# Kernel optimization log

Hardware: AMD Instinct MI355X
Metric: run time of the kernel (lower is better)

Reference implementation:

```python
import jax, jax.numpy as jnp
import numpy as np

HEADS = 16
LN_EPS = 1e-5


def setup_inputs() -> dict:
    key = jax.random.key(0)
    ks = jax.random.split(key, 12)
    B, IMG, Q, H = 8192, 2048, 768, 1024
    def init(k, shape, fan_in):
        return jax.random.normal(k, shape, dtype=jnp.float32) * (fan_in ** -0.5)
    return {
        "features1": jax.random.normal(ks[0], (B, IMG), dtype=jnp.float32),
        "features2": jax.random.normal(ks[1], (B, Q), dtype=jnp.float32),
        "W1": init(ks[2], (IMG, H), IMG),
        "b1": jnp.zeros((H,), dtype=jnp.float32),
        "W2": init(ks[3], (Q, H), Q),
        "b2": jnp.zeros((H,), dtype=jnp.float32),
        "Wqkv": init(ks[4], (H, 3 * H), H),
        "Wout": init(ks[5], (H, H), H),
        "bout": jnp.zeros((H,), dtype=jnp.float32),
        "gamma": jnp.ones((2 * H,), dtype=jnp.float32),
        "beta": jnp.zeros((2 * H,), dtype=jnp.float32),
    }


def reference(features1, features2, W1, b1, W2, b2, Wqkv, Wout, bout, gamma, beta):
    B = features1.shape[0]
    H = W1.shape[1]
    hd = H // HEADS
    scale = hd ** -0.5
    # modality projections -> [B, H] each
    f1 = features1 @ W1 + b1
    f2 = features2 @ W2 + b2
    x = jnp.stack([f1, f2], axis=1)                      # [B, 2, H]
    qkv = x @ Wqkv                                       # [B, 2, 3H]
    q, k, v = jnp.split(qkv, 3, axis=-1)
    # b n (h d) -> b h n d
    def to_heads(t):
        return t.reshape(B, 2, HEADS, hd).transpose(0, 2, 1, 3)
    q, k, v = to_heads(q) * scale, to_heads(k), to_heads(v)
    attn = jnp.einsum('bhid,bhjd->bhij', q, k)           # [B, h, 2, 2]
    attn = jax.nn.softmax(attn, axis=-1)
    out = jnp.einsum('bhij,bhjd->bhid', attn, v)         # [B, h, 2, d]
    out = out.transpose(0, 2, 1, 3).reshape(B, 2, H)     # b h n d -> b n (h d)
    out = out @ Wout + bout                              # [B, 2, H]
    flat = out.reshape(B, 2 * H)
    # LayerNorm over last dim
    mu = jnp.mean(flat, axis=-1, keepdims=True)
    var = jnp.var(flat, axis=-1, keepdims=True)
    normed = (flat - mu) * jax.lax.rsqrt(var + LN_EPS) * gamma + beta
    # dropout in eval mode = identity
    res = jnp.concatenate([f1, f2], axis=1)              # [B, 2H]
    return normed + res
```

## Files before the change

kernel.cpp:

```cpp
#include <hip/hip_runtime.h>
#include <hip/hip_bf16.h>
#include <cstdint>

typedef __attribute__((ext_vector_type(8))) short short8;
typedef __attribute__((ext_vector_type(4))) short short4v;
typedef __attribute__((ext_vector_type(4))) float floatx4;
typedef __attribute__((ext_vector_type(4))) unsigned short ushort4v;

__device__ __forceinline__ float bf2f(unsigned short u) {
    union { unsigned int u; float f; } v;
    v.u = ((unsigned int)u) << 16;
    return v.f;
}
__device__ __forceinline__ unsigned short f2bf(float f) {
    union { float f; unsigned int u; } v; v.f = f;
    unsigned int u = v.u;
    unsigned int r = (u + 0x7FFFu + ((u >> 16) & 1u)) >> 16;
    return (unsigned short)r;
}
__device__ __forceinline__ float lo_bf(unsigned int u) {
    union { unsigned int u; float f; } v; v.u = u << 16; return v.f;
}
__device__ __forceinline__ float hi_bf(unsigned int u) {
    union { unsigned int u; float f; } v; v.u = u & 0xffff0000u; return v.f;
}
__device__ __forceinline__ void gld_lds16(const void* g, void* l) {
    __builtin_amdgcn_global_load_lds(
        (const __attribute__((address_space(1))) unsigned int*)g,
        (__attribute__((address_space(3))) unsigned int*)l,
        16, 0, 0);
}

__global__ __launch_bounds__(256) void prep_kernel(
    const float* __restrict__ f1, const float* __restrict__ f2,
    unsigned short* __restrict__ f1b, unsigned short* __restrict__ f2b,
    const float* __restrict__ W1, unsigned short* __restrict__ W1t,
    const float* __restrict__ W2, unsigned short* __restrict__ W2t,
    const float* __restrict__ Wqkv, unsigned short* __restrict__ Wqkvt,
    const float* __restrict__ Wout, unsigned short* __restrict__ Woutt) {
    __shared__ float tile[64][33];
    const int b = blockIdx.x;
    const int tid = threadIdx.x;

    if (b < 5632) {
        const float* in = (b < 4096) ? f1 : f2;
        unsigned short* outp = (b < 4096) ? f1b : f2b;
        int base = ((b < 4096) ? b : (b - 4096)) * 1024 + tid;
#pragma unroll
        for (int it = 0; it < 4; it++) {
            int i = base + it * 256;
            float4 v = ((const float4*)in)[i];
            ushort4v o;
            o.x = f2bf(v.x); o.y = f2bf(v.y); o.z = f2bf(v.z); o.w = f2bf(v.w);
            ((ushort4v*)outp)[i] = o;
        }
        return;
    }

    const float* in; unsigned short* outp; int K, N, t;
    if (b < 6656)      { in = W1;   outp = W1t;   K = 2048; N = 1024; t = b - 5632; }
    else if (b < 7040) { in = W2;   outp = W2t;   K = 768;  N = 1024; t = b - 6656; }
    else if (b < 8576) { in = Wqkv; outp = Wqkvt; K = 1024; N = 3072; t = b - 7040; }
    else               { in = Wout; outp = Woutt; K = 1024; N = 1024; t = b - 8576; }
    const int ntiles = N >> 5;
    const int n0 = (t % ntiles) * 32;
    const int k0 = (t / ntiles) * 64;
    const int tx = tid & 31, tg = tid >> 5;
#pragma unroll
    for (int i = 0; i < 8; i++)
        tile[tg * 8 + i][tx] = in[(size_t)(k0 + tg * 8 + i) * N + n0 + tx];
    __syncthreads();
    const int n = tid >> 3, kc = (tid & 7) * 8;
    short8 o;
#pragma unroll
    for (int j = 0; j < 8; j++) o[j] = (short)f2bf(tile[kc + j][n]);
    *(short8*)&outp[(size_t)(n0 + n) * K + k0 + kc] = o;
}

template <bool OUT_BF16, bool HAS_BIAS>
__device__ __forceinline__ void gemm_core(const unsigned short* __restrict__ A,
                                          const unsigned short* __restrict__ Bt,
                                          void* __restrict__ Cv, const float* __restrict__ bias,
                                          int K, int ldc, int blockM, int blockN,
                                          unsigned short* As, unsigned short* Bs) {
    const int tid  = threadIdx.x;
    const int lane = tid & 63;
    const int wave = tid >> 6;
    const int wm = wave >> 1, wn = wave & 1;

    const int kx = (tid >> 3) & 3;
    const unsigned short* gA = A  + (size_t)(blockM + (tid >> 2)) * K + ((tid & 3) ^ kx) * 8;
    const unsigned short* gB = Bt + (size_t)(blockN + (tid >> 2)) * K + ((tid & 3) ^ kx) * 8;
    const size_t sK = (size_t)64 * K;
    unsigned short* lA = As + wave * 512;
    unsigned short* lB = Bs + wave * 512;

    floatx4 acc[4][4];
#pragma unroll
    for (int i = 0; i < 4; i++)
#pragma unroll
        for (int j = 0; j < 4; j++) acc[i][j] = (floatx4){0.f, 0.f, 0.f, 0.f};

    const int col  = lane & 15;
    const int quad = lane >> 4;
    const int qx = quad ^ ((col >> 1) & 3);
    const int aoff32 = (wm * 64 + col) * 32 + qx * 8;
    const int boff32 = (wn * 64 + col) * 32 + qx * 8;

    const int kIters = K >> 6;
    for (int kt = 0; kt < kIters; ++kt) {
        const size_t ko = (size_t)kt * 64;
        gld_lds16(gA + ko,           lA);
        gld_lds16(gA + sK + ko,      lA + 2048);
        gld_lds16(gA + 32 + ko,      lA + 4096);
        gld_lds16(gA + sK + 32 + ko, lA + 6144);
        gld_lds16(gB + ko,           lB);
        gld_lds16(gB + sK + ko,      lB + 2048);
        gld_lds16(gB + 32 + ko,      lB + 4096);
        gld_lds16(gB + sK + 32 + ko, lB + 6144);
        __syncthreads();

#pragma unroll
        for (int hh = 0; hh < 2; hh++) {
            short8 a[4];
#pragma unroll
            for (int i = 0; i < 4; i++) a[i] = *(const short8*)&As[hh * 4096 + aoff32 + i * 512];
#pragma unroll
            for (int j = 0; j < 4; j++) {
                short8 bj = *(const short8*)&Bs[hh * 4096 + boff32 + j * 512];
#pragma unroll
                for (int i = 0; i < 4; i++)
                    acc[i][j] = __builtin_amdgcn_mfma_f32_16x16x32_bf16(a[i], bj, acc[i][j], 0, 0, 0);
            }
        }
        __syncthreads();
    }

#pragma unroll
    for (int i = 0; i < 4; i++) {
#pragma unroll
        for (int j = 0; j < 4; j++) {
#pragma unroll
            for (int r = 0; r < 4; r++) {
                int row = blockM + wm * 64 + i * 16 + quad * 4 + r;
                int cn  = blockN + wn * 64 + j * 16 + col;
                float v = acc[i][j][r];
                if (HAS_BIAS) v += bias[cn];
                if (OUT_BF16) ((unsigned short*)Cv)[(size_t)row * ldc + cn] = f2bf(v);
                else          ((float*)Cv)[(size_t)row * ldc + cn] = v;
            }
        }
    }
}

__global__ __launch_bounds__(256, 3)
void gemm_f12(const unsigned short* __restrict__ f1b, const unsigned short* __restrict__ W1t,
              const float* __restrict__ b1,
              const unsigned short* __restrict__ f2b, const unsigned short* __restrict__ W2t,
              const float* __restrict__ b2, unsigned short* __restrict__ xb) {
    __shared__ alignas(16) unsigned short As[8192];
    __shared__ alignas(16) unsigned short Bs[8192];
    const int blockM = blockIdx.x * 128;
    const int blockN = blockIdx.y * 128;
    if (blockIdx.z == 0)
        gemm_core<true, true>(f1b, W1t, (void*)xb, b1, 2048, 2048, blockM, blockN, As, Bs);
    else
        gemm_core<true, true>(f2b, W2t, (void*)(xb + 1024), b2, 768, 2048, blockM, blockN, As, Bs);
}

__global__ __launch_bounds__(256, 3)
void gemm_proj(const unsigned short* __restrict__ attn, const unsigned short* __restrict__ Woutt,
               const float* __restrict__ bout, unsigned short* __restrict__ projb) {
    __shared__ alignas(16) unsigned short As[8192];
    __shared__ alignas(16) unsigned short Bs[8192];
    gemm_core<true, true>(attn, Woutt, (void*)projb, bout, 1024, 1024,
                          blockIdx.x * 128, blockIdx.y * 128, As, Bs);
}

#define QKV_LDS_BYTES 116736
#define T2_ST 264
__global__ __launch_bounds__(512, 2)
void gemm_qkv_attn2(const unsigned short* __restrict__ A, const unsigned short* __restrict__ Bt,
                    unsigned short* __restrict__ attn_out) {
    extern __shared__ __align__(16) char smem[];
    unsigned short* buf0 = (unsigned short*)smem;
    unsigned short* buf1 = (unsigned short*)(smem + 57344);
    unsigned short* T2   = (unsigned short*)smem;
    float* wsm = (float*)(smem + 114688);

    const int tid  = threadIdx.x;
    const int lane = tid & 63;
    const int wave = tid >> 6;
    const int wm = wave >> 1;
    const int wn = wave & 1;
    const int g = blockIdx.x;
    const int h = g >> 6;
    const int blockM = (g & 63) * 256;
    const int K = 1024;

    const int srow = tid >> 3;
    const int schunk = (tid & 7) ^ (srow & 7);
    const unsigned short* gA = A  + (size_t)(blockM + srow) * K + schunk * 8;
    const unsigned short* gB = Bt + (size_t)(h * 64 + srow) * K + schunk * 8;
    const int sdst = wave * 512;

#define STAGE_A(bufp, koff) do { \
    gld_lds16(gA + (koff),          (bufp) + sdst);          \
    gld_lds16(gA + 65536 + (koff),  (bufp) + 4096 + sdst);   \
    gld_lds16(gA + 131072 + (koff), (bufp) + 8192 + sdst);   \
    gld_lds16(gA + 196608 + (koff), (bufp) + 12288 + sdst); } while (0)
#define STAGE_B(bufp, koff) do { \
    gld_lds16(gB + (koff),           (bufp) + 16384 + sdst);         \
    gld_lds16(gB + 1048576 + (koff), (bufp) + 16384 + 4096 + sdst);  \
    gld_lds16(gB + 2097152 + (koff), (bufp) + 16384 + 8192 + sdst); } while (0)

    floatx4 acc[4][6];
#pragma unroll
    for (int i = 0; i < 4; i++)
#pragma unroll
        for (int j = 0; j < 6; j++) acc[i][j] = (floatx4){0.f, 0.f, 0.f, 0.f};

    const int col  = lane & 15;
    const int quad = lane >> 4;
    const int ch0  = (quad ^ (col & 7)) * 8;
    int aoff[4], boff[6];
#pragma unroll
    for (int i = 0; i < 4; i++) aoff[i] = (wm * 64 + i * 16 + col) * 64 + ch0;
#pragma unroll
    for (int j = 0; j < 6; j++) boff[j] = 16384 + (wn * 96 + j * 16 + col) * 64 + ch0;

    STAGE_A(buf0, 0);
    STAGE_B(buf0, 0);

    for (int kt = 0; kt < 16; ++kt) {
        unsigned short* cur = (kt & 1) ? buf1 : buf0;
        unsigned short* nxt = (kt & 1) ? buf0 : buf1;
        const int kn = (kt + 1) * 64;
        __syncthreads();

        short8 a0[4], b0v[3];
#pragma unroll
        for (int i = 0; i < 4; i++) a0[i] = *(const short8*)&cur[aoff[i]];
#pragma unroll
        for (int j = 0; j < 3; j++) b0v[j] = *(const short8*)&cur[boff[j]];
        if (kt < 15) { STAGE_A(nxt, kn); }
        __builtin_amdgcn_sched_barrier(0);
        __builtin_amdgcn_s_barrier();
        asm volatile("s_waitcnt lgkmcnt(0)" ::: "memory");
        __builtin_amdgcn_sched_barrier(0);
        __builtin_amdgcn_s_setprio(1);
#pragma unroll
        for (int j = 0; j < 3; j++)
#pragma unroll
            for (int i = 0; i < 4; i++)
                acc[i][j] = __builtin_amdgcn_mfma_f32_16x16x32_bf16(a0[i], b0v[j], acc[i][j], 0, 0, 0);
        __builtin_amdgcn_s_setprio(0);
        __builtin_amdgcn_sched_barrier(0);
        __builtin_amdgcn_s_barrier();

        short8 b1v[3];
#pragma unroll
        for (int j = 0; j < 3; j++) b1v[j] = *(const short8*)&cur[boff[3 + j]];
        if (kt < 15) { STAGE_B(nxt, kn); }
        __builtin_amdgcn_sched_barrier(0);
        __builtin_amdgcn_s_barrier();
        asm volatile("s_waitcnt lgkmcnt(0)" ::: "memory");
        __builtin_amdgcn_sched_barrier(0);
        __builtin_amdgcn_s_setprio(1);
#pragma unroll
        for (int j = 0; j < 3; j++)
#pragma unroll
            for (int i = 0; i < 4; i++)
                acc[i][3 + j] = __builtin_amdgcn_mfma_f32_16x16x32_bf16(a0[i], b1v[j], acc[i][3 + j], 0, 0, 0);
        __builtin_amdgcn_s_setprio(0);
        __builtin_amdgcn_sched_barrier(0);
        __builtin_amdgcn_s_barrier();

        short8 a1[4], b2v[3];
#pragma unroll
        for (int i = 0; i < 4; i++) a1[i] = *(const short8*)&cur[aoff[i] ^ 32];
#pragma unroll
        for (int j = 0; j < 3; j++) b2v[j] = *(const short8*)&cur[boff[j] ^ 32];
        __builtin_amdgcn_sched_barrier(0);
        __builtin_amdgcn_s_barrier();
        asm volatile("s_waitcnt lgkmcnt(0)" ::: "memory");
        __builtin_amdgcn_sched_barrier(0);
        __builtin_amdgcn_s_setprio(1);
#pragma unroll
        for (int j = 0; j < 3; j++)
#pragma unroll
            for (int i = 0; i < 4; i++)
                acc[i][j] = __builtin_amdgcn_mfma_f32_16x16x32_bf16(a1[i], b2v[j], acc[i][j], 0, 0, 0);
        __builtin_amdgcn_s_setprio(0);
        __builtin_amdgcn_sched_barrier(0);
        __builtin_amdgcn_s_barrier();

        short8 b3v[3];
#pragma unroll
        for (int j = 0; j < 3; j++) b3v[j] = *(const short8*)&cur[boff[3 + j] ^ 32];
        __builtin_amdgcn_sched_barrier(0);
        __builtin_amdgcn_s_barrier();
        asm volatile("s_waitcnt lgkmcnt(0)" ::: "memory");
        __builtin_amdgcn_sched_barrier(0);
        __builtin_amdgcn_s_setprio(1);
#pragma unroll
        for (int j = 0; j < 3; j++)
#pragma unroll
            for (int i = 0; i < 4; i++)
                acc[i][3 + j] = __builtin_amdgcn_mfma_f32_16x16x32_bf16(a1[i], b3v[j], acc[i][3 + j], 0, 0, 0);
        __builtin_amdgcn_s_setprio(0);
    }
    __syncthreads();
#undef STAGE_A
#undef STAGE_B

#pragma unroll
    for (int i = 0; i < 4; i++) {
#pragma unroll
        for (int j = 0; j < 6; j++) {
            int c  = wn * 96 + j * 16 + col;
            int r0 = wm * 64 + i * 16 + quad * 4;
            short4v pk;
            pk.x = (short)f2bf(acc[i][j][0]);
            pk.y = (short)f2bf(acc[i][j][1]);
            pk.z = (short)f2bf(acc[i][j][2]);
            pk.w = (short)f2bf(acc[i][j][3]);
            *(short4v*)&T2[c * T2_ST + r0] = pk;
        }
    }
    __syncthreads();

    if (tid < 128) {
        const int ib = tid;
        float s00 = 0.f, s01 = 0.f, s10 = 0.f, s11 = 0.f;
#pragma unroll 8
        for (int d = 0; d < 64; d++) {
            unsigned int qp = *(const unsigned int*)&T2[d * T2_ST + 2 * ib];
            unsigned int kp = *(const unsigned int*)&T2[(64 + d) * T2_ST + 2 * ib];
            float q0 = lo_bf(qp), q1 = hi_bf(qp);
            float k0 = lo_bf(kp), k1 = hi_bf(kp);
            s00 += q0 * k0; s01 += q0 * k1;
            s10 += q1 * k0; s11 += q1 * k1;
        }
        const float sc = 0.125f;
        s00 *= sc; s01 *= sc; s10 *= sc; s11 *= sc;
        float m0 = fmaxf(s00, s01), m1 = fmaxf(s10, s11);
        float e00 = __expf(s00 - m0), e01 = __expf(s01 - m0);
        float e10 = __expf(s10 - m1), e11 = __expf(s11 - m1);
        float i0 = 1.f / (e00 + e01), i1 = 1.f / (e10 + e11);
        wsm[ib * 4 + 0] = e00 * i0; wsm[ib * 4 + 1] = e01 * i0;
        wsm[ib * 4 + 2] = e10 * i1; wsm[ib * 4 + 3] = e11 * i1;
    }
    __syncthreads();

#pragma unroll
    for (int gg = 0; gg < 4; gg++) {
        int chunk = gg * 512 + tid;
        int r = chunk >> 3;
        int dc = (chunk & 7) * 8;
        int ib = r >> 1, n = r & 1;
        float w0 = wsm[ib * 4 + n * 2 + 0];
        float w1 = wsm[ib * 4 + n * 2 + 1];
        short8 o;
#pragma unroll
        for (int dd = 0; dd < 8; dd++) {
            unsigned int vp = *(const unsigned int*)&T2[(128 + dc + dd) * T2_ST + 2 * ib];
            o[dd] = (short)f2bf(w0 * lo_bf(vp) + w1 * hi_bf(vp));
        }
        *(short8*)&attn_out[(size_t)(blockM + r) * 1024 + h * 64 + dc] = o;
    }
}

__global__ __launch_bounds__(256) void ln_res_kernel(const unsigned short* __restrict__ proj,
                                                     const unsigned short* __restrict__ xres,
                                                     const float* __restrict__ gamma,
                                                     const float* __restrict__ beta,
                                                     float* __restrict__ out) {
    const int b = blockIdx.x;
    const int tid = threadIdx.x;
    const size_t base = (size_t)b * 2048;
    short8 p8 = ((const short8*)(proj + base))[tid];
    float pv[8];
#pragma unroll
    for (int e = 0; e < 8; e++) pv[e] = bf2f((unsigned short)p8[e]);
    float s = 0.f, ss = 0.f;
#pragma unroll
    for (int e = 0; e < 8; e++) { s += pv[e]; ss += pv[e] * pv[e]; }
#pragma unroll
    for (int off = 32; off > 0; off >>= 1) {
        s  += __shfl_xor(s, off);
        ss += __shfl_xor(ss, off);
    }
    __shared__ float red[8];
    const int wave = tid >> 6;
    if ((tid & 63) == 0) { red[wave] = s; red[4 + wave] = ss; }
    __syncthreads();
    s  = red[0] + red[1] + red[2] + red[3];
    ss = red[4] + red[5] + red[6] + red[7];
    const float mean = s * (1.0f / 2048.0f);
    const float var  = ss * (1.0f / 2048.0f) - mean * mean;
    const float rstd = rsqrtf(var + 1e-5f);

    const float4* g4 = (const float4*)gamma;
    const float4* b4 = (const float4*)beta;
    float4 g0 = g4[2 * tid], g1 = g4[2 * tid + 1];
    float4 be0 = b4[2 * tid], be1 = b4[2 * tid + 1];
    short8 r8 = ((const short8*)(xres + base))[tid];
    float4 o0, o1;
    o0.x = (pv[0] - mean) * rstd * g0.x + be0.x + bf2f((unsigned short)r8[0]);
    o0.y = (pv[1] - mean) * rstd * g0.y + be0.y + bf2f((unsigned short)r8[1]);
    o0.z = (pv[2] - mean) * rstd * g0.z + be0.z + bf2f((unsigned short)r8[2]);
    o0.w = (pv[3] - mean) * rstd * g0.w + be0.w + bf2f((unsigned short)r8[3]);
    o1.x = (pv[4] - mean) * rstd * g1.x + be1.x + bf2f((unsigned short)r8[4]);
    o1.y = (pv[5] - mean) * rstd * g1.y + be1.y + bf2f((unsigned short)r8[5]);
    o1.z = (pv[6] - mean) * rstd * g1.z + be1.z + bf2f((unsigned short)r8[6]);
    o1.w = (pv[7] - mean) * rstd * g1.w + be1.w + bf2f((unsigned short)r8[7]);
    float4* op = (float4*)(out + base);
    op[2 * tid] = o0;
    op[2 * tid + 1] = o1;
}

extern "C" void kernel_launch(void* const* d_in, const int* in_sizes, int n_in,
                              void* d_out, int out_size, void* d_ws, size_t ws_size,
                              hipStream_t stream) {
    (void)in_sizes; (void)n_in; (void)out_size; (void)ws_size;
    const float* features1 = (const float*)d_in[0];
    const float* features2 = (const float*)d_in[1];
    const float* W1   = (const float*)d_in[2];
    const float* b1   = (const float*)d_in[3];
    const float* W2   = (const float*)d_in[4];
    const float* b2   = (const float*)d_in[5];
    const float* Wqkv = (const float*)d_in[6];
    const float* Wout = (const float*)d_in[7];
    const float* bout = (const float*)d_in[8];
    const float* gamma = (const float*)d_in[9];
    const float* beta  = (const float*)d_in[10];
    float* out = (float*)d_out;

    static bool qkv2_init = false;
    if (!qkv2_init) {
        (void)hipFuncSetAttribute((const void*)gemm_qkv_attn2,
                                  hipFuncAttributeMaxDynamicSharedMemorySize,
                                  QKV_LDS_BYTES);
        qkv2_init = true;
    }

    char* ws = (char*)d_ws;
    unsigned short* f1b   = (unsigned short*)(ws);
    unsigned short* f2b   = (unsigned short*)(ws + 33554432);
    unsigned short* W1t   = (unsigned short*)(ws + 46137344);
    unsigned short* W2t   = (unsigned short*)(ws + 50331648);
    unsigned short* Wqkvt = (unsigned short*)(ws + 51904512);
    unsigned short* Woutt = (unsigned short*)(ws + 58195968);
    unsigned short* xb    = (unsigned short*)(ws + 60293120);
    unsigned short* attn  = (unsigned short*)(ws + 93847552);
    unsigned short* projb = (unsigned short*)(ws + 127401984);

    prep_kernel<<<9088, 256, 0, stream>>>(features1, features2, f1b, f2b,
                                          W1, W1t, W2, W2t, Wqkv, Wqkvt, Wout, Woutt);
    gemm_f12<<<dim3(64, 8, 2), 256, 0, stream>>>(f1b, W1t, b1, f2b, W2t, b2, xb);
    gemm_qkv_attn2<<<1024, 512, QKV_LDS_BYTES, stream>>>(xb, Wqkvt, attn);
    gemm_proj<<<dim3(128, 8), 256, 0, stream>>>(attn, Woutt, bout, projb);
    ln_res_kernel<<<8192, 256, 0, stream>>>(projb, xb, gamma, beta, out);
}
```

Measured before the change: 389.1 us.

## Split QKV-attention K tile into halves with finer-grained prefetch and vmcnt waits

The fused QKV+attention GEMM now stores each 64-wide K tile as two 32-wide half-tiles with a new XOR swizzle. Global-to-LDS staging is split into four smaller chunks interleaved across the four MFMA phases, with explicit vmcnt waits replacing the leading __syncthreads. The intent is to overlap global loads with compute more evenly and reduce LDS bank conflicts. LDS grows to 128 KB per block, which with two blocks per CU may exceed capacity and reduce occupancy. The projection GEMMs also raise launch_bounds min-blocks from 3 to 4, which may cause register pressure.

```diff
diff --git a/kernel.cpp b/kernel.cpp
--- a/kernel.cpp
+++ b/kernel.cpp
@@ -153,7 +153,7 @@
     }
 }
 
-__global__ __launch_bounds__(256, 3)
+__global__ __launch_bounds__(256, 4)
 void gemm_f12(const unsigned short* __restrict__ f1b, const unsigned short* __restrict__ W1t,
               const float* __restrict__ b1,
               const unsigned short* __restrict__ f2b, const unsigned short* __restrict__ W2t,
@@ -168,7 +168,7 @@
         gemm_core<true, true>(f2b, W2t, (void*)(xb + 1024), b2, 768, 2048, blockM, blockN, As, Bs);
 }
 
-__global__ __launch_bounds__(256, 3)
+__global__ __launch_bounds__(256, 4)
 void gemm_proj(const unsigned short* __restrict__ attn, const unsigned short* __restrict__ Woutt,
                const float* __restrict__ bout, unsigned short* __restrict__ projb) {
     __shared__ alignas(16) unsigned short As[8192];
@@ -177,42 +177,50 @@
                           blockIdx.x * 128, blockIdx.y * 128, As, Bs);
 }
 
-#define QKV_LDS_BYTES 116736
+#define QKV_LDS_BYTES 131072
 #define T2_ST 264
 __global__ __launch_bounds__(512, 2)
-void gemm_qkv_attn2(const unsigned short* __restrict__ A, const unsigned short* __restrict__ Bt,
+void gemm_qkv_attn8(const unsigned short* __restrict__ A, const unsigned short* __restrict__ Bt,
                     unsigned short* __restrict__ attn_out) {
     extern __shared__ __align__(16) char smem[];
     unsigned short* buf0 = (unsigned short*)smem;
-    unsigned short* buf1 = (unsigned short*)(smem + 57344);
+    unsigned short* buf1 = buf0 + 32768;
     unsigned short* T2   = (unsigned short*)smem;
-    float* wsm = (float*)(smem + 114688);
+    float* wsm = (float*)(smem + 101376);
 
     const int tid  = threadIdx.x;
     const int lane = tid & 63;
     const int wave = tid >> 6;
-    const int wm = wave >> 1;
-    const int wn = wave & 1;
     const int g = blockIdx.x;
     const int h = g >> 6;
     const int blockM = (g & 63) * 256;
+    const int wm = wave >> 1;
+    const int wn = wave & 1;
     const int K = 1024;
 
-    const int srow = tid >> 3;
-    const int schunk = (tid & 7) ^ (srow & 7);
-    const unsigned short* gA = A  + (size_t)(blockM + srow) * K + schunk * 8;
-    const unsigned short* gB = Bt + (size_t)(h * 64 + srow) * K + schunk * 8;
-    const int sdst = wave * 512;
-
-#define STAGE_A(bufp, koff) do { \
-    gld_lds16(gA + (koff),          (bufp) + sdst);          \
-    gld_lds16(gA + 65536 + (koff),  (bufp) + 4096 + sdst);   \
-    gld_lds16(gA + 131072 + (koff), (bufp) + 8192 + sdst);   \
-    gld_lds16(gA + 196608 + (koff), (bufp) + 12288 + sdst); } while (0)
-#define STAGE_B(bufp, koff) do { \
-    gld_lds16(gB + (koff),           (bufp) + 16384 + sdst);         \
-    gld_lds16(gB + 1048576 + (koff), (bufp) + 16384 + 4096 + sdst);  \
-    gld_lds16(gB + 2097152 + (koff), (bufp) + 16384 + 8192 + sdst); } while (0)
+    const int srow = tid >> 2;
+    const int sch  = ((tid & 3) ^ ((tid >> 3) & 3)) * 8;
+    const unsigned short* gA = A + (size_t)(blockM + srow) * K + sch;
+    const int bt   = tid & 255;
+    const int brow = bt >> 2;
+    const int qk_row = (tid < 256) ? (h * 64 + brow) : (1024 + h * 64 + brow);
+    const int v_row  = 2048 + h * 64 + brow;
+    const unsigned short* gBqk = Bt + (size_t)qk_row * K + sch;
+    const unsigned short* gBv  = Bt + (size_t)v_row  * K + sch;
+    const int wo = wave * 512;
+
+#define ST_A0(p, ko) do { \
+    gld_lds16(gA + (ko),               (p) + wo);            \
+    gld_lds16(gA + 131072 + (ko),      (p) + 4096 + wo); } while (0)
+#define ST_A1(p, ko) do { \
+    gld_lds16(gA + 32 + (ko),          (p) + 8192 + wo);     \
+    gld_lds16(gA + 131072 + 32 + (ko), (p) + 12288 + wo); } while (0)
+#define ST_B0(p, ko) do { \
+    gld_lds16(gBqk + (ko),             (p) + 16384 + wo);    \
+    gld_lds16(gBv + (ko),              (p) + 20480 + wo); } while (0)
+#define ST_B1(p, ko) do { \
+    gld_lds16(gBqk + 32 + (ko),        (p) + 24576 + wo);    \
+    gld_lds16(gBv + 32 + (ko),         (p) + 28672 + wo); } while (0)
 
     floatx4 acc[4][6];
 #pragma unroll
@@ -222,30 +230,33 @@
 
     const int col  = lane & 15;
     const int quad = lane >> 4;
-    const int ch0  = (quad ^ (col & 7)) * 8;
+    const int qx = quad ^ ((col >> 1) & 3);
     int aoff[4], boff[6];
 #pragma unroll
-    for (int i = 0; i < 4; i++) aoff[i] = (wm * 64 + i * 16 + col) * 64 + ch0;
-#pragma unroll
-    for (int j = 0; j < 6; j++) boff[j] = 16384 + (wn * 96 + j * 16 + col) * 64 + ch0;
-
-    STAGE_A(buf0, 0);
-    STAGE_B(buf0, 0);
+    for (int i = 0; i < 4; i++) aoff[i] = (wm * 64 + i * 16 + col) * 32 + qx * 8;
+#pragma unroll
+    for (int j = 0; j < 6; j++) boff[j] = 16384 + (wn * 96 + j * 16 + col) * 32 + qx * 8;
+
+    ST_A0(buf0, 0); ST_A1(buf0, 0); ST_B0(buf0, 0); ST_B1(buf0, 0);
 
     for (int kt = 0; kt < 16; ++kt) {
         unsigned short* cur = (kt & 1) ? buf1 : buf0;
         unsigned short* nxt = (kt & 1) ? buf0 : buf1;
-        const int kn = (kt + 1) * 64;
-        __syncthreads();
-
+        const size_t kn = (size_t)(kt + 1) * 64;
+
+        if (kt < 15) {
+            ST_A0(nxt, kn);
+            asm volatile("s_waitcnt vmcnt(2)" ::: "memory");
+        } else {
+            asm volatile("s_waitcnt vmcnt(0)" ::: "memory");
+        }
+        __builtin_amdgcn_sched_barrier(0);
+        __builtin_amdgcn_s_barrier();
         short8 a0[4], b0v[3];
 #pragma unroll
         for (int i = 0; i < 4; i++) a0[i] = *(const short8*)&cur[aoff[i]];
 #pragma unroll
         for (int j = 0; j < 3; j++) b0v[j] = *(const short8*)&cur[boff[j]];
-        if (kt < 15) { STAGE_A(nxt, kn); }
-        __builtin_amdgcn_sched_barrier(0);
-        __builtin_amdgcn_s_barrier();
         asm volatile("s_waitcnt lgkmcnt(0)" ::: "memory");
         __builtin_amdgcn_sched_barrier(0);
         __builtin_amdgcn_s_setprio(1);
@@ -261,7 +272,7 @@
         short8 b1v[3];
 #pragma unroll
         for (int j = 0; j < 3; j++) b1v[j] = *(const short8*)&cur[boff[3 + j]];
-        if (kt < 15) { STAGE_B(nxt, kn); }
+        if (kt < 15) { ST_A1(nxt, kn); }
         __builtin_amdgcn_sched_barrier(0);
         __builtin_amdgcn_s_barrier();
         asm volatile("s_waitcnt lgkmcnt(0)" ::: "memory");
@@ -278,9 +289,10 @@
 
         short8 a1[4], b2v[3];
 #pragma unroll
-        for (int i = 0; i < 4; i++) a1[i] = *(const short8*)&cur[aoff[i] ^ 32];
-#pragma unroll
-        for (int j = 0; j < 3; j++) b2v[j] = *(const short8*)&cur[boff[j] ^ 32];
+        for (int i = 0; i < 4; i++) a1[i] = *(const short8*)&cur[8192 + aoff[i]];
+#pragma unroll
+        for (int j = 0; j < 3; j++) b2v[j] = *(const short8*)&cur[8192 + boff[j]];
+        if (kt < 15) { ST_B0(nxt, kn); }
         __builtin_amdgcn_sched_barrier(0);
         __builtin_amdgcn_s_barrier();
         asm volatile("s_waitcnt lgkmcnt(0)" ::: "memory");
@@ -297,7 +309,8 @@
 
         short8 b3v[3];
 #pragma unroll
-        for (int j = 0; j < 3; j++) b3v[j] = *(const short8*)&cur[boff[3 + j] ^ 32];
+        for (int j = 0; j < 3; j++) b3v[j] = *(const short8*)&cur[8192 + boff[3 + j]];
+        if (kt < 15) { ST_B1(nxt, kn); }
         __builtin_amdgcn_sched_barrier(0);
         __builtin_amdgcn_s_barrier();
         asm volatile("s_waitcnt lgkmcnt(0)" ::: "memory");
@@ -309,10 +322,14 @@
             for (int i = 0; i < 4; i++)
                 acc[i][3 + j] = __builtin_amdgcn_mfma_f32_16x16x32_bf16(a1[i], b3v[j], acc[i][3 + j], 0, 0, 0);
         __builtin_amdgcn_s_setprio(0);
-    }
+        __builtin_amdgcn_sched_barrier(0);
+        __builtin_amdgcn_s_barrier();
+    }
+#undef ST_A0
+#undef ST_A1
+#undef ST_B0
+#undef ST_B1
     __syncthreads();
-#undef STAGE_A
-#undef STAGE_B
 
 #pragma unroll
     for (int i = 0; i < 4; i++) {
@@ -437,12 +454,12 @@
     const float* beta  = (const float*)d_in[10];
     float* out = (float*)d_out;
 
-    static bool qkv2_init = false;
-    if (!qkv2_init) {
-        (void)hipFuncSetAttribute((const void*)gemm_qkv_attn2,
+    static bool qkv8_init = false;
+    if (!qkv8_init) {
+        (void)hipFuncSetAttribute((const void*)gemm_qkv_attn8,
                                   hipFuncAttributeMaxDynamicSharedMemorySize,
                                   QKV_LDS_BYTES);
-        qkv2_init = true;
+        qkv8_init = true;
     }
 
     char* ws = (char*)d_ws;
@@ -459,7 +476,7 @@
     prep_kernel<<<9088, 256, 0, stream>>>(features1, features2, f1b, f2b,
                                           W1, W1t, W2, W2t, Wqkv, Wqkvt, Wout, Woutt);
     gemm_f12<<<dim3(64, 8, 2), 256, 0, stream>>>(f1b, W1t, b1, f2b, W2t, b2, xb);
-    gemm_qkv_attn2<<<1024, 512, QKV_LDS_BYTES, stream>>>(xb, Wqkvt, attn);
+    gemm_qkv_attn8<<<1024, 512, QKV_LDS_BYTES, stream>>>(xb, Wqkvt, attn);
     gemm_proj<<<dim3(128, 8), 256, 0, stream>>>(attn, Woutt, bout, projb);
     ln_res_kernel<<<8192, 256, 0, stream>>>(projb, xb, gamma, beta, out);
 }
```

New measurement: 373.3 us. 4.1% less time.
